# Kernel optimization log

Hardware: AMD Instinct MI355X
Metric: run time of the kernel (lower is better)

The kernel has to match this reference:

```python
import jax, jax.numpy as jnp
import numpy as np

N = 100000      # nodes
E = 800000      # directed edges
D_IN = 128      # input features (n_inputs)
HIDDEN = 128    # conf['model']['hidden_size']
D_OUT = 2       # conv2 output classes


def setup_inputs() -> dict:
    key = jax.random.key(0)
    k0, k1, k2, k3 = jax.random.split(key, 4)
    x = jax.random.normal(k0, (N, D_IN), dtype=jnp.float32)
    edge_index = jax.random.randint(k1, (2, E), 0, N, dtype=jnp.int32)
    # Glorot-style init for GCNConv weights, zero bias (PyG defaults)
    s1 = float(np.sqrt(6.0 / (D_IN + HIDDEN)))
    s2 = float(np.sqrt(6.0 / (HIDDEN + D_OUT)))
    W1 = jax.random.uniform(k2, (D_IN, HIDDEN), jnp.float32, -s1, s1)
    b1 = jnp.zeros((HIDDEN,), jnp.float32)
    W2 = jax.random.uniform(k3, (HIDDEN, D_OUT), jnp.float32, -s2, s2)
    b2 = jnp.zeros((D_OUT,), jnp.float32)
    return {"x": x, "edge_index": edge_index, "W1": W1, "b1": b1, "W2": W2, "b2": b2}


def gcn_conv(x, src, dst, W, b):
    """PyG GCNConv: add self-loops, symmetric deg^-1/2 A deg^-1/2 normalization."""
    n = x.shape[0]
    h = x @ W                                                   # [N, F_out]
    ones_e = jnp.ones((src.shape[0],), h.dtype)
    # degree with self-loops (init to 1)
    deg = jnp.ones((n,), h.dtype).at[dst].add(ones_e)           # [N]
    dinv = 1.0 / jnp.sqrt(deg)
    norm = (dinv[src] * dinv[dst])[:, None]                     # [E, 1]
    # self-loop contribution: norm_ii = dinv_i^2; then scatter edge messages
    out = (h * (dinv * dinv)[:, None]).at[dst].add(h[src] * norm)
    return out + b


def reference(x, edge_index, W1, b1, W2, b2):
    src, dst = edge_index[0], edge_index[1]
    h = jax.nn.relu(gcn_conv(x, src, dst, W1, b1))
    return gcn_conv(h, src, dst, W2, b2)                        # [N, 2]
```

## Files before the change

kernel.cpp:

```cpp
#include <hip/hip_runtime.h>
#include <hip/hip_bf16.h>


#define D1 128
#define BSH 9
#define BSZ (1 << BSH)
#define CHA 4096

typedef __attribute__((ext_vector_type(8))) short short8;
typedef __attribute__((ext_vector_type(4))) float floatx4;

__device__ __forceinline__ unsigned short f2bf(float f) {
    unsigned u = __float_as_uint(f);
    u += 0x7fff + ((u >> 16) & 1);
    return (unsigned short)(u >> 16);
}
__device__ __forceinline__ float bflo(unsigned u) { return __uint_as_float(u << 16); }
__device__ __forceinline__ float bfhi(unsigned u) { return __uint_as_float(u & 0xffff0000u); }

__global__ void k_init(const float* __restrict__ W1, unsigned short* __restrict__ W1t,
                       int* __restrict__ bcount) {
    int i = blockIdx.x * 256 + threadIdx.x;
    if (i < 256) bcount[i] = 0;
    if (i < D1 * D1) {
        int c = i >> 7, k = i & 127;
        W1t[c * D1 + k] = f2bf(W1[k * D1 + c]);
    }
}

__global__ __launch_bounds__(256) void k_bcount(const int* __restrict__ dst,
                                                int* __restrict__ bcount,
                                                int E, int nbuck) {
    __shared__ int h[256];
    int t = threadIdx.x;
    h[t] = 0;
    __syncthreads();
    for (int i = blockIdx.x * 256 + t; i < E; i += gridDim.x * 256)
        atomicAdd(&h[dst[i] >> BSH], 1);
    __syncthreads();
    if (t < nbuck && h[t]) atomicAdd(&bcount[t], h[t]);
}

__global__ __launch_bounds__(256) void k_bscan(const int* __restrict__ bcount,
                                               int* __restrict__ bbase,
                                               int* __restrict__ bcur,
                                               int* __restrict__ rowptr,
                                               int nbuck, int N, int E) {
    __shared__ int sd[256];
    int t = threadIdx.x;
    int v = (t < nbuck) ? bcount[t] : 0;
    sd[t] = v;
    __syncthreads();
    for (int off = 1; off < 256; off <<= 1) {
        int x = (t >= off) ? sd[t - off] : 0;
        __syncthreads();
        sd[t] += x;
        __syncthreads();
    }
    int excl = sd[t] - v;
    if (t < nbuck) { bbase[t] = excl; bcur[t] = excl; }
    if (t == 0) {
        bbase[nbuck] = E;
        rowptr[N] = E;
    }
}

__global__ __launch_bounds__(256) void k_binA(
    const int* __restrict__ src, const int* __restrict__ dst,
    int* __restrict__ bcur, unsigned* __restrict__ packed, int E, int nbuck)
{
    __shared__ int hist[256];
    __shared__ int cur[256];
    const int t = threadIdx.x;
    const int e0 = blockIdx.x * CHA;
    const int e1 = min(e0 + CHA, E);

    for (int i = t; i < nbuck; i += 256) hist[i] = 0;
    __syncthreads();
    for (int i = e0 + t; i < e1; i += 256)
        atomicAdd(&hist[dst[i] >> BSH], 1);
    __syncthreads();
    for (int i = t; i < nbuck; i += 256)
        cur[i] = (hist[i] > 0) ? atomicAdd(&bcur[i], hist[i]) : 0;
    __syncthreads();
    for (int i = e0 + t; i < e1; i += 256) {
        int d = dst[i];
        int b = d >> BSH;
        int pos = atomicAdd(&cur[b], 1);
        packed[pos] = ((unsigned)src[i] << BSH) | (unsigned)(d & (BSZ - 1));
    }
}

__global__ __launch_bounds__(512) void k_binB(
    const int* __restrict__ bbase, const unsigned* __restrict__ packed,
    int* __restrict__ rowptr, float* __restrict__ dinv,
    int* __restrict__ esrc, int* __restrict__ order, int N)
{
    __shared__ int lh[BSZ];
    __shared__ int sd[BSZ];
    __shared__ int lcur[BSZ];
    __shared__ int dbin[64];
    __shared__ int dcur[64];

    const int t = threadIdx.x;
    const int s = blockIdx.x << BSH;
    const int n = min(BSZ, N - s);
    const int base = bbase[blockIdx.x];
    const int cnt = bbase[blockIdx.x + 1] - base;

    lh[t] = 0;
    if (t < 64) dbin[t] = 0;
    __syncthreads();
    for (int i = t; i < cnt; i += 512)
        atomicAdd(&lh[packed[base + i] & (BSZ - 1)], 1);
    __syncthreads();

    sd[t] = lh[t];
    __syncthreads();
    for (int off = 1; off < BSZ; off <<= 1) {
        int x = (t >= off) ? sd[t - off] : 0;
        __syncthreads();
        sd[t] += x;
        __syncthreads();
    }
    int excl = sd[t] - lh[t];
    if (t < n) {
        rowptr[s + t] = base + excl;
        dinv[s + t] = rsqrtf(1.0f + (float)lh[t]);
        atomicAdd(&dbin[63 - min(lh[t], 63)], 1);
    }
    lcur[t] = excl;
    __syncthreads();

    for (int i = t; i < cnt; i += 512) {
        unsigned p = packed[base + i];
        int ld = (int)(p & (BSZ - 1));
        int pos = atomicAdd(&lcur[ld], 1);
        esrc[base + pos] = (int)(p >> BSH);
    }

    __syncthreads();
    if (t < 64) sd[t] = dbin[t];
    __syncthreads();
    for (int off = 1; off < 64; off <<= 1) {
        int x = (t >= off && t < 64) ? sd[t - off] : 0;
        __syncthreads();
        if (t < 64) sd[t] += x;
        __syncthreads();
    }
    if (t < 64) dcur[t] = sd[t] - dbin[t];
    __syncthreads();
    if (t < n) {
        int b = 63 - min(lh[t], 63);
        int pos = atomicAdd(&dcur[b], 1);
        order[s + pos] = s + t;
    }
}

#define BMM 64
__global__ __launch_bounds__(256) void k_gemm1(
    const float* __restrict__ x, const unsigned short* __restrict__ W1t,
    const float* __restrict__ dinv, unsigned short* __restrict__ h1s, int N)
{
    __shared__ unsigned short Xs[BMM][136];
    __shared__ unsigned short Ws[D1][136];

    const int t = threadIdx.x;
    const int row0 = blockIdx.x * BMM;

#pragma unroll
    for (int i = 0; i < 8; ++i) {
        int idx = t + 256 * i;
        int r = idx >> 4, c8 = idx & 15;
        short8 v = ((const short8*)W1t)[r * 16 + c8];
        *(short8*)&Ws[r][c8 * 8] = v;
    }
#pragma unroll
    for (int i = 0; i < 4; ++i) {
        int idx = t + 256 * i;
        int r = idx >> 4, c8 = idx & 15;
        int row = row0 + r;
        short8 v8 = (short8)0;
        if (row < N) {
            const float* p = x + (size_t)row * D1 + c8 * 8;
            float4 f0 = *(const float4*)p;
            float4 f1 = *(const float4*)(p + 4);
            v8[0] = (short)f2bf(f0.x); v8[1] = (short)f2bf(f0.y);
            v8[2] = (short)f2bf(f0.z); v8[3] = (short)f2bf(f0.w);
            v8[4] = (short)f2bf(f1.x); v8[5] = (short)f2bf(f1.y);
            v8[6] = (short)f2bf(f1.z); v8[7] = (short)f2bf(f1.w);
        }
        *(short8*)&Xs[r][c8 * 8] = v8;
    }
    __syncthreads();

    const int w = t >> 6;
    const int l = t & 63;
    const int m = l & 15;
    const int q = l >> 4;

    floatx4 acc[8];
#pragma unroll
    for (int c = 0; c < 8; ++c) acc[c] = (floatx4)0.0f;

#pragma unroll
    for (int ks = 0; ks < 4; ++ks) {
        short8 a = *(const short8*)&Xs[16 * w + m][ks * 32 + q * 8];
#pragma unroll
        for (int c = 0; c < 8; ++c) {
            short8 b = *(const short8*)&Ws[c * 16 + m][ks * 32 + q * 8];
            acc[c] = __builtin_amdgcn_mfma_f32_16x16x32_bf16(a, b, acc[c], 0, 0, 0);
        }
    }

    __syncthreads();

#pragma unroll
    for (int r = 0; r < 4; ++r) {
        int rt = 16 * w + q * 4 + r;
        int row = row0 + rt;
        float di = (row < N) ? dinv[row] : 0.f;
#pragma unroll
        for (int c = 0; c < 8; ++c)
            Xs[rt][c * 16 + m] = f2bf(acc[c][r] * di);
    }
    __syncthreads();

#pragma unroll
    for (int i = 0; i < 4; ++i) {
        int idx = t + 256 * i;
        int r = idx >> 4, c8 = idx & 15;
        int row = row0 + r;
        if (row < N)
            *(short8*)&h1s[(size_t)row * D1 + c8 * 8] = *(const short8*)&Xs[r][c8 * 8];
    }
}

#define ACC8(A, v) \
    A[0] += bflo(v.x); A[1] += bfhi(v.x); \
    A[2] += bflo(v.y); A[3] += bfhi(v.y); \
    A[4] += bflo(v.z); A[5] += bfhi(v.z); \
    A[6] += bflo(v.w); A[7] += bfhi(v.w);

__global__ __launch_bounds__(256) void k_agg1_gemm2(
    const int* __restrict__ rowptr, const int* __restrict__ esrc,
    const int* __restrict__ order,
    const float* __restrict__ dinv, const unsigned short* __restrict__ h1s,
    const float* __restrict__ b1, const float* __restrict__ W2,
    float* __restrict__ h2s, int N)
{
    int gid = blockIdx.x * 256 + threadIdx.x;
    int grp = gid >> 4;
    if (grp >= N) return;
    int node = order[grp];
    int lane = gid & 15;

    const uint4* h1v = (const uint4*)h1s;

    uint4 u = h1v[(size_t)node * 16 + lane];
    float accA[8], accB[8];
    accA[0] = bflo(u.x); accA[1] = bfhi(u.x);
    accA[2] = bflo(u.y); accA[3] = bfhi(u.y);
    accA[4] = bflo(u.z); accA[5] = bfhi(u.z);
    accA[6] = bflo(u.w); accA[7] = bfhi(u.w);
#pragma unroll
    for (int j = 0; j < 8; ++j) accB[j] = 0.f;

    int beg = rowptr[node], end = rowptr[node + 1];
    int e = beg;
    for (; e + 7 < end; e += 8) {
        int s0 = esrc[e],     s1 = esrc[e + 1], s2 = esrc[e + 2], s3 = esrc[e + 3];
        int s4 = esrc[e + 4], s5 = esrc[e + 5], s6 = esrc[e + 6], s7 = esrc[e + 7];
        uint4 v0 = h1v[(size_t)s0 * 16 + lane];
        uint4 v1 = h1v[(size_t)s1 * 16 + lane];
        uint4 v2 = h1v[(size_t)s2 * 16 + lane];
        uint4 v3 = h1v[(size_t)s3 * 16 + lane];
        uint4 v4 = h1v[(size_t)s4 * 16 + lane];
        uint4 v5 = h1v[(size_t)s5 * 16 + lane];
        uint4 v6 = h1v[(size_t)s6 * 16 + lane];
        uint4 v7 = h1v[(size_t)s7 * 16 + lane];
        ACC8(accA, v0) ACC8(accB, v1) ACC8(accA, v2) ACC8(accB, v3)
        ACC8(accA, v4) ACC8(accB, v5) ACC8(accA, v6) ACC8(accB, v7)
    }
    if (e + 3 < end) {
        int s0 = esrc[e], s1 = esrc[e + 1], s2 = esrc[e + 2], s3 = esrc[e + 3];
        uint4 v0 = h1v[(size_t)s0 * 16 + lane];
        uint4 v1 = h1v[(size_t)s1 * 16 + lane];
        uint4 v2 = h1v[(size_t)s2 * 16 + lane];
        uint4 v3 = h1v[(size_t)s3 * 16 + lane];
        ACC8(accA, v0) ACC8(accB, v1) ACC8(accA, v2) ACC8(accB, v3)
        e += 4;
    }
    for (; e < end; ++e) {
        uint4 v = h1v[(size_t)esrc[e] * 16 + lane];
        ACC8(accB, v)
    }

    float di = dinv[node];
    const float4* b1v = (const float4*)b1;
    float4 bbA = b1v[lane * 2 + 0];
    float4 bbB = b1v[lane * 2 + 1];
    float a[8];
    a[0] = fmaxf((accA[0] + accB[0]) * di + bbA.x, 0.f);
    a[1] = fmaxf((accA[1] + accB[1]) * di + bbA.y, 0.f);
    a[2] = fmaxf((accA[2] + accB[2]) * di + bbA.z, 0.f);
    a[3] = fmaxf((accA[3] + accB[3]) * di + bbA.w, 0.f);
    a[4] = fmaxf((accA[4] + accB[4]) * di + bbB.x, 0.f);
    a[5] = fmaxf((accA[5] + accB[5]) * di + bbB.y, 0.f);
    a[6] = fmaxf((accA[6] + accB[6]) * di + bbB.z, 0.f);
    a[7] = fmaxf((accA[7] + accB[7]) * di + bbB.w, 0.f);

    const float4* W2v = (const float4*)W2;
    float p0 = 0.f, p1 = 0.f;
#pragma unroll
    for (int j2 = 0; j2 < 4; ++j2) {
        float4 wv = W2v[lane * 4 + j2];
        p0 += a[j2 * 2] * wv.x + a[j2 * 2 + 1] * wv.z;
        p1 += a[j2 * 2] * wv.y + a[j2 * 2 + 1] * wv.w;
    }

#pragma unroll
    for (int off = 8; off > 0; off >>= 1) {
        p0 += __shfl_xor(p0, off);
        p1 += __shfl_xor(p1, off);
    }
    if (lane == 0) {
        h2s[(size_t)node * 2 + 0] = p0 * di;
        h2s[(size_t)node * 2 + 1] = p1 * di;
    }
}

__global__ void k_gather2(const int* __restrict__ rowptr, const int* __restrict__ esrc,
                          const float* __restrict__ h2s, const float* __restrict__ dinv,
                          const float* __restrict__ b2, float* __restrict__ out, int N)
{
    int i = blockIdx.x * 256 + threadIdx.x;
    if (i >= N) return;
    const float2* h2v = (const float2*)h2s;
    float2 h = h2v[i];
    float o0a = h.x, o1a = h.y;
    float o0b = 0.f, o1b = 0.f;
    int beg = rowptr[i], end = rowptr[i + 1];
    int e = beg;
    for (; e + 7 < end; e += 8) {
        int s0 = esrc[e],     s1 = esrc[e + 1], s2 = esrc[e + 2], s3 = esrc[e + 3];
        int s4 = esrc[e + 4], s5 = esrc[e + 5], s6 = esrc[e + 6], s7 = esrc[e + 7];
        float2 v0 = h2v[s0], v1 = h2v[s1], v2 = h2v[s2], v3 = h2v[s3];
        float2 v4 = h2v[s4], v5 = h2v[s5], v6 = h2v[s6], v7 = h2v[s7];
        o0a += v0.x + v2.x + v4.x + v6.x; o1a += v0.y + v2.y + v4.y + v6.y;
        o0b += v1.x + v3.x + v5.x + v7.x; o1b += v1.y + v3.y + v5.y + v7.y;
    }
    for (; e < end; ++e) {
        float2 v = h2v[esrc[e]];
        o0b += v.x; o1b += v.y;
    }
    float di = dinv[i];
    ((float2*)out)[i] = make_float2((o0a + o0b) * di + b2[0], (o1a + o1b) * di + b2[1]);
}

extern "C" void kernel_launch(void* const* d_in, const int* in_sizes, int n_in,
                              void* d_out, int out_size, void* d_ws, size_t ws_size,
                              hipStream_t stream)
{
    const float* x  = (const float*)d_in[0];
    const int*   ei = (const int*)d_in[1];
    const float* W1 = (const float*)d_in[2];
    const float* b1 = (const float*)d_in[3];
    const float* W2 = (const float*)d_in[4];
    const float* b2 = (const float*)d_in[5];
    float* out = (float*)d_out;

    const int N = in_sizes[0] / D1;
    const int E = in_sizes[1] / 2;
    const int* src = ei;
    const int* dst = ei + E;

    char* w = (char*)d_ws;
    auto alloc = [&](size_t bytes) -> char* {
        char* r = w;
        w += (bytes + 63) & ~(size_t)63;
        return r;
    };
    unsigned short* h1s = (unsigned short*)alloc((size_t)N * D1 * 2);
    unsigned short* W1t = (unsigned short*)alloc((size_t)D1 * D1 * 2);
    float* h2s    = (float*)alloc((size_t)N * 2 * 4);
    float* dinv   = (float*)alloc((size_t)N * 4);
    int*   rowptr = (int*)alloc((size_t)(N + 4) * 4);
    int*   order  = (int*)alloc((size_t)N * 4);
    int*   bcount = (int*)alloc(256 * 4);
    int*   bbase  = (int*)alloc(260 * 4);
    int*   bcur   = (int*)alloc(256 * 4);
    unsigned* packed = (unsigned*)alloc((size_t)E * 4);
    int*   esrc   = (int*)alloc((size_t)E * 4);

    const int nbuck = (N + BSZ - 1) >> BSH;

    k_init  <<<(D1 * D1 + 255) / 256, 256, 0, stream>>>(W1, W1t, bcount);
    k_bcount<<<256, 256, 0, stream>>>(dst, bcount, E, nbuck);
    k_bscan <<<1, 256, 0, stream>>>(bcount, bbase, bcur, rowptr, nbuck, N, E);
    k_binA  <<<(E + CHA - 1) / CHA, 256, 0, stream>>>(src, dst, bcur, packed, E, nbuck);
    k_binB  <<<nbuck, 512, 0, stream>>>(bbase, packed, rowptr, dinv, esrc, order, N);

    k_gemm1<<<(N + BMM - 1) / BMM, 256, 0, stream>>>(x, W1t, dinv, h1s, N);

    k_agg1_gemm2<<<(N * 16 + 255) / 256, 256, 0, stream>>>(rowptr, esrc, order, dinv, h1s, b1, W2, h2s, N);

    k_gather2<<<(N + 255) / 256, 256, 0, stream>>>(rowptr, esrc, h2s, dinv, b2, out, N);
}
```

Measured before the change: 196.1 us.

## Use wave-shuffle scans, zero-padded sentinel row for predicated gather, smaller binning chunk

Replaces the LDS Hillis-Steele scans in the bucket scan and per-bucket CSR build with wavefront shuffle scans plus a small cross-wave combine, which cuts the number of barriers. The gather loops in both aggregation kernels now always issue 8 loads per iteration. Out-of-range slots point at a new zeroed sentinel row N in h1s and h2s, which removes the scalar tail loops and lowers divergence. The binning chunk size is also halved to launch more blocks. Padded iterations spend extra load bandwidth on the sentinel row, which stays cached.

```diff
diff --git a/kernel.cpp b/kernel.cpp
--- a/kernel.cpp
+++ b/kernel.cpp
@@ -5,7 +5,7 @@
 #define D1 128
 #define BSH 9
 #define BSZ (1 << BSH)
-#define CHA 4096
+#define CHA 2048
 
 typedef __attribute__((ext_vector_type(8))) short short8;
 typedef __attribute__((ext_vector_type(4))) float floatx4;
@@ -19,9 +19,12 @@
 __device__ __forceinline__ float bfhi(unsigned u) { return __uint_as_float(u & 0xffff0000u); }
 
 __global__ void k_init(const float* __restrict__ W1, unsigned short* __restrict__ W1t,
-                       int* __restrict__ bcount) {
+                       int* __restrict__ bcount, unsigned short* __restrict__ h1s,
+                       float* __restrict__ h2s, int N) {
     int i = blockIdx.x * 256 + threadIdx.x;
     if (i < 256) bcount[i] = 0;
+    if (i < D1) h1s[(size_t)N * D1 + i] = 0;
+    if (i < 2)  h2s[(size_t)N * 2 + i] = 0.f;
     if (i < D1 * D1) {
         int c = i >> 7, k = i & 127;
         W1t[c * D1 + k] = f2bf(W1[k * D1 + c]);
@@ -46,18 +49,28 @@
                                                int* __restrict__ bcur,
                                                int* __restrict__ rowptr,
                                                int nbuck, int N, int E) {
-    __shared__ int sd[256];
+    __shared__ int wsum[4];
     int t = threadIdx.x;
     int v = (t < nbuck) ? bcount[t] : 0;
-    sd[t] = v;
-    __syncthreads();
-    for (int off = 1; off < 256; off <<= 1) {
-        int x = (t >= off) ? sd[t - off] : 0;
-        __syncthreads();
-        sd[t] += x;
-        __syncthreads();
-    }
-    int excl = sd[t] - v;
+    int inc = v;
+#pragma unroll
+    for (int off = 1; off < 64; off <<= 1) {
+        int u = __shfl_up(inc, off);
+        if ((t & 63) >= off) inc += u;
+    }
+    if ((t & 63) == 63) wsum[t >> 6] = inc;
+    __syncthreads();
+    if (t < 4) {
+        int w = wsum[t];
+#pragma unroll
+        for (int off = 1; off < 4; off <<= 1) {
+            int u = __shfl_up(w, off, 4);
+            if ((t & 3) >= off) w += u;
+        }
+        wsum[t] = w;
+    }
+    __syncthreads();
+    int excl = ((t >> 6) ? wsum[(t >> 6) - 1] : 0) + inc - v;
     if (t < nbuck) { bbase[t] = excl; bcur[t] = excl; }
     if (t == 0) {
         bbase[nbuck] = E;
@@ -97,8 +110,8 @@
     int* __restrict__ esrc, int* __restrict__ order, int N)
 {
     __shared__ int lh[BSZ];
-    __shared__ int sd[BSZ];
     __shared__ int lcur[BSZ];
+    __shared__ int wsum[8];
     __shared__ int dbin[64];
     __shared__ int dcur[64];
 
@@ -115,19 +128,31 @@
         atomicAdd(&lh[packed[base + i] & (BSZ - 1)], 1);
     __syncthreads();
 
-    sd[t] = lh[t];
-    __syncthreads();
-    for (int off = 1; off < BSZ; off <<= 1) {
-        int x = (t >= off) ? sd[t - off] : 0;
-        __syncthreads();
-        sd[t] += x;
-        __syncthreads();
-    }
-    int excl = sd[t] - lh[t];
+    int v = lh[t];
+    int inc = v;
+#pragma unroll
+    for (int off = 1; off < 64; off <<= 1) {
+        int u = __shfl_up(inc, off);
+        if ((t & 63) >= off) inc += u;
+    }
+    if ((t & 63) == 63) wsum[t >> 6] = inc;
+    __syncthreads();
+    if (t < 8) {
+        int w = wsum[t];
+#pragma unroll
+        for (int off = 1; off < 8; off <<= 1) {
+            int u = __shfl_up(w, off, 8);
+            if ((t & 7) >= off) w += u;
+        }
+        wsum[t] = w;
+    }
+    __syncthreads();
+    int excl = ((t >> 6) ? wsum[(t >> 6) - 1] : 0) + inc - v;
+
     if (t < n) {
         rowptr[s + t] = base + excl;
-        dinv[s + t] = rsqrtf(1.0f + (float)lh[t]);
-        atomicAdd(&dbin[63 - min(lh[t], 63)], 1);
+        dinv[s + t] = rsqrtf(1.0f + (float)v);
+        atomicAdd(&dbin[63 - min(v, 63)], 1);
     }
     lcur[t] = excl;
     __syncthreads();
@@ -140,18 +165,19 @@
     }
 
     __syncthreads();
-    if (t < 64) sd[t] = dbin[t];
-    __syncthreads();
-    for (int off = 1; off < 64; off <<= 1) {
-        int x = (t >= off && t < 64) ? sd[t - off] : 0;
-        __syncthreads();
-        if (t < 64) sd[t] += x;
-        __syncthreads();
-    }
-    if (t < 64) dcur[t] = sd[t] - dbin[t];
+    if (t < 64) {
+        int dv = dbin[t];
+        int dinc = dv;
+#pragma unroll
+        for (int off = 1; off < 64; off <<= 1) {
+            int u = __shfl_up(dinc, off);
+            if (t >= off) dinc += u;
+        }
+        dcur[t] = dinc - dv;
+    }
     __syncthreads();
     if (t < n) {
-        int b = 63 - min(lh[t], 63);
+        int b = 63 - min(v, 63);
         int pos = atomicAdd(&dcur[b], 1);
         order[s + pos] = s + t;
     }
@@ -267,10 +293,15 @@
     for (int j = 0; j < 8; ++j) accB[j] = 0.f;
 
     int beg = rowptr[node], end = rowptr[node + 1];
-    int e = beg;
-    for (; e + 7 < end; e += 8) {
-        int s0 = esrc[e],     s1 = esrc[e + 1], s2 = esrc[e + 2], s3 = esrc[e + 3];
-        int s4 = esrc[e + 4], s5 = esrc[e + 5], s6 = esrc[e + 6], s7 = esrc[e + 7];
+    for (int e = beg; e < end; e += 8) {
+        int s0 = (e + 0 < end) ? esrc[e + 0] : N;
+        int s1 = (e + 1 < end) ? esrc[e + 1] : N;
+        int s2 = (e + 2 < end) ? esrc[e + 2] : N;
+        int s3 = (e + 3 < end) ? esrc[e + 3] : N;
+        int s4 = (e + 4 < end) ? esrc[e + 4] : N;
+        int s5 = (e + 5 < end) ? esrc[e + 5] : N;
+        int s6 = (e + 6 < end) ? esrc[e + 6] : N;
+        int s7 = (e + 7 < end) ? esrc[e + 7] : N;
         uint4 v0 = h1v[(size_t)s0 * 16 + lane];
         uint4 v1 = h1v[(size_t)s1 * 16 + lane];
         uint4 v2 = h1v[(size_t)s2 * 16 + lane];
@@ -281,19 +312,6 @@
         uint4 v7 = h1v[(size_t)s7 * 16 + lane];
         ACC8(accA, v0) ACC8(accB, v1) ACC8(accA, v2) ACC8(accB, v3)
         ACC8(accA, v4) ACC8(accB, v5) ACC8(accA, v6) ACC8(accB, v7)
-    }
-    if (e + 3 < end) {
-        int s0 = esrc[e], s1 = esrc[e + 1], s2 = esrc[e + 2], s3 = esrc[e + 3];
-        uint4 v0 = h1v[(size_t)s0 * 16 + lane];
-        uint4 v1 = h1v[(size_t)s1 * 16 + lane];
-        uint4 v2 = h1v[(size_t)s2 * 16 + lane];
-        uint4 v3 = h1v[(size_t)s3 * 16 + lane];
-        ACC8(accA, v0) ACC8(accB, v1) ACC8(accA, v2) ACC8(accB, v3)
-        e += 4;
-    }
-    for (; e < end; ++e) {
-        uint4 v = h1v[(size_t)esrc[e] * 16 + lane];
-        ACC8(accB, v)
     }
 
     float di = dinv[node];
@@ -341,18 +359,19 @@
     float o0a = h.x, o1a = h.y;
     float o0b = 0.f, o1b = 0.f;
     int beg = rowptr[i], end = rowptr[i + 1];
-    int e = beg;
-    for (; e + 7 < end; e += 8) {
-        int s0 = esrc[e],     s1 = esrc[e + 1], s2 = esrc[e + 2], s3 = esrc[e + 3];
-        int s4 = esrc[e + 4], s5 = esrc[e + 5], s6 = esrc[e + 6], s7 = esrc[e + 7];
+    for (int e = beg; e < end; e += 8) {
+        int s0 = (e + 0 < end) ? esrc[e + 0] : N;
+        int s1 = (e + 1 < end) ? esrc[e + 1] : N;
+        int s2 = (e + 2 < end) ? esrc[e + 2] : N;
+        int s3 = (e + 3 < end) ? esrc[e + 3] : N;
+        int s4 = (e + 4 < end) ? esrc[e + 4] : N;
+        int s5 = (e + 5 < end) ? esrc[e + 5] : N;
+        int s6 = (e + 6 < end) ? esrc[e + 6] : N;
+        int s7 = (e + 7 < end) ? esrc[e + 7] : N;
         float2 v0 = h2v[s0], v1 = h2v[s1], v2 = h2v[s2], v3 = h2v[s3];
         float2 v4 = h2v[s4], v5 = h2v[s5], v6 = h2v[s6], v7 = h2v[s7];
         o0a += v0.x + v2.x + v4.x + v6.x; o1a += v0.y + v2.y + v4.y + v6.y;
         o0b += v1.x + v3.x + v5.x + v7.x; o1b += v1.y + v3.y + v5.y + v7.y;
-    }
-    for (; e < end; ++e) {
-        float2 v = h2v[esrc[e]];
-        o0b += v.x; o1b += v.y;
     }
     float di = dinv[i];
     ((float2*)out)[i] = make_float2((o0a + o0b) * di + b2[0], (o1a + o1b) * di + b2[1]);
@@ -381,9 +400,9 @@
         w += (bytes + 63) & ~(size_t)63;
         return r;
     };
-    unsigned short* h1s = (unsigned short*)alloc((size_t)N * D1 * 2);
+    unsigned short* h1s = (unsigned short*)alloc((size_t)(N + 1) * D1 * 2);
     unsigned short* W1t = (unsigned short*)alloc((size_t)D1 * D1 * 2);
-    float* h2s    = (float*)alloc((size_t)N * 2 * 4);
+    float* h2s    = (float*)alloc((size_t)(N + 1) * 2 * 4);
     float* dinv   = (float*)alloc((size_t)N * 4);
     int*   rowptr = (int*)alloc((size_t)(N + 4) * 4);
     int*   order  = (int*)alloc((size_t)N * 4);
@@ -395,7 +414,7 @@
 
     const int nbuck = (N + BSZ - 1) >> BSH;
 
-    k_init  <<<(D1 * D1 + 255) / 256, 256, 0, stream>>>(W1, W1t, bcount);
+    k_init  <<<(D1 * D1 + 255) / 256, 256, 0, stream>>>(W1, W1t, bcount, h1s, h2s, N);
     k_bcount<<<256, 256, 0, stream>>>(dst, bcount, E, nbuck);
     k_bscan <<<1, 256, 0, stream>>>(bcount, bbase, bcur, rowptr, nbuck, N, E);
     k_binA  <<<(E + CHA - 1) / CHA, 256, 0, stream>>>(src, dst, bcur, packed, E, nbuck);
```

Result: faster. 189.3 us (-3.4%).
